# Kernel tuning notes

Measured on AMD Instinct MI355X. Metric: run time of the kernel, lower is better.

Reference implementation:

```python
import jax, jax.numpy as jnp
import numpy as np

N, D = 1024, 256


def setup_inputs() -> dict:
    key = jax.random.key(0)
    k1, k2, k3, k4, k5 = jax.random.split(key, 5)
    s1 = 1.0 / np.sqrt(2 * D)  # fan_in of first linear
    s2 = 1.0 / np.sqrt(D)      # fan_in of second linear
    return {
        "nodes": jax.random.normal(k1, (N, D), dtype=jnp.float32),
        "W1": jax.random.normal(k2, (D, 2 * D), dtype=jnp.float32) * s1,
        "b1": jax.random.normal(k3, (D,), dtype=jnp.float32) * s1,
        "W2": jax.random.normal(k4, (1, D), dtype=jnp.float32) * s2,
        "b2": jax.random.normal(k5, (1,), dtype=jnp.float32) * s2,
    }


def reference(nodes, W1, b1, W2, b2):
    # Original: pair = cat([n_i, n_j], -1); A = sigmoid(Linear2(relu(Linear1(pair))))
    # Algebraically: Linear1(cat(n_i, n_j)) = n_i @ Wa^T + n_j @ Wb^T + b1
    d = nodes.shape[1]
    Wa, Wb = W1[:, :d], W1[:, d:]
    a = nodes @ Wa.T  # (N, D) row-side projection
    b = nodes @ Wb.T  # (N, D) col-side projection
    h = jax.nn.relu(a[:, None, :] + b[None, :, :] + b1)  # (N, N, D)
    logits = jnp.einsum("ijd,d->ij", h, W2[0]) + b2[0]   # (N, N)
    return jax.nn.sigmoid(logits)
```

## Files before the change

### kernel.cpp

```cpp
#include <hip/hip_runtime.h>
#include <math.h>

#define N_NODES 1024
#define DIM     256

__global__ __launch_bounds__(256) void k1_gemm(
    const float* __restrict__ nodes, const float* __restrict__ W1,
    const float* __restrict__ b1, float* __restrict__ At, float* __restrict__ Bt)
{
    __shared__ float nt[64][34];
    __shared__ float wa[64][34];
    __shared__ float wb[64][34];

    const int i0 = (blockIdx.x & 31) * 32;
    const int d0 = (blockIdx.x >> 5) * 32;
    const int t  = threadIdx.x;
    const int tx = t & 15;
    const int ty = t >> 4;

    float aA00=0.f,aA01=0.f,aA10=0.f,aA11=0.f;
    float aB00=0.f,aB01=0.f,aB10=0.f,aB11=0.f;

    const int r = t >> 3;
    const int c = (t & 7) * 8;

    for (int k0 = 0; k0 < DIM; k0 += 64) {
        const float* sn = nodes + (i0 + r) * DIM + k0 + c;
        float4 n0 = *(const float4*)(sn);
        float4 n1 = *(const float4*)(sn + 4);
        const float* sa = W1 + (d0 + r) * (2 * DIM) + k0 + c;
        float4 a0 = *(const float4*)(sa);
        float4 a1 = *(const float4*)(sa + 4);
        const float* sb = sa + DIM;
        float4 q0 = *(const float4*)(sb);
        float4 q1 = *(const float4*)(sb + 4);

        __syncthreads();

        nt[c+0][r]=n0.x; nt[c+1][r]=n0.y; nt[c+2][r]=n0.z; nt[c+3][r]=n0.w;
        nt[c+4][r]=n1.x; nt[c+5][r]=n1.y; nt[c+6][r]=n1.z; nt[c+7][r]=n1.w;
        wa[c+0][r]=a0.x; wa[c+1][r]=a0.y; wa[c+2][r]=a0.z; wa[c+3][r]=a0.w;
        wa[c+4][r]=a1.x; wa[c+5][r]=a1.y; wa[c+6][r]=a1.z; wa[c+7][r]=a1.w;
        wb[c+0][r]=q0.x; wb[c+1][r]=q0.y; wb[c+2][r]=q0.z; wb[c+3][r]=q0.w;
        wb[c+4][r]=q1.x; wb[c+5][r]=q1.y; wb[c+6][r]=q1.z; wb[c+7][r]=q1.w;

        __syncthreads();

        #pragma unroll 16
        for (int k = 0; k < 64; ++k) {
            float2 av = *(const float2*)&nt[k][tx*2];
            float2 pv = *(const float2*)&wa[k][ty*2];
            float2 qv = *(const float2*)&wb[k][ty*2];
            aA00 += av.x*pv.x; aA01 += av.x*pv.y;
            aA10 += av.y*pv.x; aA11 += av.y*pv.y;
            aB00 += av.x*qv.x; aB01 += av.x*qv.y;
            aB10 += av.y*qv.x; aB11 += av.y*qv.y;
        }
    }

    const int i = i0 + tx*2;
    const int d = d0 + ty*2;
    const float bb0 = b1[d], bb1 = b1[d+1];
    At[(d  )*N_NODES + i  ] = aA00 + bb0;
    At[(d+1)*N_NODES + i  ] = aA01 + bb1;
    At[(d  )*N_NODES + i+1] = aA10 + bb0;
    At[(d+1)*N_NODES + i+1] = aA11 + bb1;
    Bt[(d  )*N_NODES + i  ] = aB00;
    Bt[(d+1)*N_NODES + i  ] = aB01;
    Bt[(d  )*N_NODES + i+1] = aB10;
    Bt[(d+1)*N_NODES + i+1] = aB11;
}

__global__ __launch_bounds__(256) void k2_pair(
    const float* __restrict__ At, const float* __restrict__ Bt,
    const float* __restrict__ W2, const float* __restrict__ b2,
    float* __restrict__ out)
{
    __shared__ float As[64][68];
    __shared__ float Bs[64][68];
    __shared__ float w2s[DIM];

    const int i0 = (blockIdx.x & 15) * 64;
    const int j0 = (blockIdx.x >> 4) * 64;
    const int t  = threadIdx.x;
    const int tx = t & 15;
    const int ty = t >> 4;

    w2s[t] = W2[t];

    float acc[4][4] = {{0.f,0.f,0.f,0.f},{0.f,0.f,0.f,0.f},
                       {0.f,0.f,0.f,0.f},{0.f,0.f,0.f,0.f}};

    const int r = t >> 2;
    const int c = (t & 3) * 16;

    for (int dc = 0; dc < DIM; dc += 64) {
        const float* sa = At + (dc + r) * N_NODES + i0 + c;
        const float* sb = Bt + (dc + r) * N_NODES + j0 + c;
        float4 va0 = *(const float4*)(sa);
        float4 va1 = *(const float4*)(sa + 4);
        float4 va2 = *(const float4*)(sa + 8);
        float4 va3 = *(const float4*)(sa + 12);
        float4 vb0 = *(const float4*)(sb);
        float4 vb1 = *(const float4*)(sb + 4);
        float4 vb2 = *(const float4*)(sb + 8);
        float4 vb3 = *(const float4*)(sb + 12);

        __syncthreads();

        *(float4*)&As[r][c   ] = va0;
        *(float4*)&As[r][c+ 4] = va1;
        *(float4*)&As[r][c+ 8] = va2;
        *(float4*)&As[r][c+12] = va3;
        *(float4*)&Bs[r][c   ] = vb0;
        *(float4*)&Bs[r][c+ 4] = vb1;
        *(float4*)&Bs[r][c+ 8] = vb2;
        *(float4*)&Bs[r][c+12] = vb3;

        __syncthreads();

        #pragma unroll 16
        for (int k = 0; k < 64; ++k) {
            float4 a4 = *(const float4*)&As[k][ty*4];
            float4 b4 = *(const float4*)&Bs[k][tx*4];
            float  w  = w2s[dc + k];
            acc[0][0] += fmaxf(a4.x + b4.x, 0.f) * w;
            acc[0][1] += fmaxf(a4.x + b4.y, 0.f) * w;
            acc[0][2] += fmaxf(a4.x + b4.z, 0.f) * w;
            acc[0][3] += fmaxf(a4.x + b4.w, 0.f) * w;
            acc[1][0] += fmaxf(a4.y + b4.x, 0.f) * w;
            acc[1][1] += fmaxf(a4.y + b4.y, 0.f) * w;
            acc[1][2] += fmaxf(a4.y + b4.z, 0.f) * w;
            acc[1][3] += fmaxf(a4.y + b4.w, 0.f) * w;
            acc[2][0] += fmaxf(a4.z + b4.x, 0.f) * w;
            acc[2][1] += fmaxf(a4.z + b4.y, 0.f) * w;
            acc[2][2] += fmaxf(a4.z + b4.z, 0.f) * w;
            acc[2][3] += fmaxf(a4.z + b4.w, 0.f) * w;
            acc[3][0] += fmaxf(a4.w + b4.x, 0.f) * w;
            acc[3][1] += fmaxf(a4.w + b4.y, 0.f) * w;
            acc[3][2] += fmaxf(a4.w + b4.z, 0.f) * w;
            acc[3][3] += fmaxf(a4.w + b4.w, 0.f) * w;
        }
    }

    const float bb = b2[0];
    #pragma unroll
    for (int m = 0; m < 4; ++m) {
        float4 o;
        float x0 = acc[m][0] + bb;
        float x1 = acc[m][1] + bb;
        float x2 = acc[m][2] + bb;
        float x3 = acc[m][3] + bb;
        o.x = 1.0f / (1.0f + __expf(-x0));
        o.y = 1.0f / (1.0f + __expf(-x1));
        o.z = 1.0f / (1.0f + __expf(-x2));
        o.w = 1.0f / (1.0f + __expf(-x3));
        *(float4*)&out[(i0 + ty*4 + m) * N_NODES + j0 + tx*4] = o;
    }
}

extern "C" void kernel_launch(void* const* d_in, const int* in_sizes, int n_in,
                              void* d_out, int out_size, void* d_ws, size_t ws_size,
                              hipStream_t stream) {
    const float* nodes = (const float*)d_in[0];
    const float* W1    = (const float*)d_in[1];
    const float* b1    = (const float*)d_in[2];
    const float* W2    = (const float*)d_in[3];
    const float* b2    = (const float*)d_in[4];
    float* out = (float*)d_out;

    float* At = (float*)d_ws;
    float* Bt = At + DIM * N_NODES;

    k1_gemm<<<256, 256, 0, stream>>>(nodes, W1, b1, At, Bt);
    k2_pair<<<256, 256, 0, stream>>>(At, Bt, W2, b2, out);
}
```

Before: 102.2 us.

## Rewrite pair kernel with packed-FP32 inline asm and direct global loads

The pair kernel drops its shared-memory staging and barriers and reads At/Bt columns straight from global memory (L1/L2), with smaller 2x4 per-thread tiles and 32x64 blocks. The grid doubles to 512 blocks to fill more CUs. Inline asm issues v_pk_add_f32 and v_pk_fma_f32 so two adds and two FMAs go out per instruction, cutting the VALU issue count of the add-relu-FMA inner loop. The cost is lower register-level reuse per thread and more global/cache traffic per FLOP.

Measured after the change: 150.5 us. +47.2%, slower.

```diff
diff --git a/kernel.cpp b/kernel.cpp
--- a/kernel.cpp
+++ b/kernel.cpp
@@ -3,6 +3,33 @@
 
 #define N_NODES 1024
 #define DIM     256
+
+typedef float f32x2 __attribute__((ext_vector_type(2)));
+typedef float f32x4 __attribute__((ext_vector_type(4)));
+
+__device__ __forceinline__ f32x2 pk_add_blo(f32x2 a, f32x2 b) {
+    f32x2 d;
+    asm("v_pk_add_f32 %0, %1, %2 op_sel:[0,0] op_sel_hi:[0,1]"
+        : "=v"(d) : "v"(a), "v"(b));
+    return d;
+}
+__device__ __forceinline__ f32x2 pk_add_bhi(f32x2 a, f32x2 b) {
+    f32x2 d;
+    asm("v_pk_add_f32 %0, %1, %2 op_sel:[1,0] op_sel_hi:[1,1]"
+        : "=v"(d) : "v"(a), "v"(b));
+    return d;
+}
+__device__ __forceinline__ void pk_fma_wlo(f32x2& acc, f32x2 h, f32x2 w) {
+    asm("v_pk_fma_f32 %0, %1, %2, %0 op_sel:[0,0,0] op_sel_hi:[1,0,1]"
+        : "+v"(acc) : "v"(h), "v"(w));
+}
+__device__ __forceinline__ void pk_fma_whi(f32x2& acc, f32x2 h, f32x2 w) {
+    asm("v_pk_fma_f32 %0, %1, %2, %0 op_sel:[0,1,0] op_sel_hi:[1,1,1]"
+        : "+v"(acc) : "v"(h), "v"(w));
+}
+__device__ __forceinline__ f32x2 relu2(f32x2 x) {
+    return __builtin_elementwise_max(x, (f32x2)0.0f);
+}
 
 __global__ __launch_bounds__(256) void k1_gemm(
     const float* __restrict__ nodes, const float* __restrict__ W1,
@@ -71,92 +98,64 @@
     Bt[(d+1)*N_NODES + i+1] = aB11;
 }
 
-__global__ __launch_bounds__(256) void k2_pair(
+__global__ __launch_bounds__(256, 2) void k2_pair(
     const float* __restrict__ At, const float* __restrict__ Bt,
     const float* __restrict__ W2, const float* __restrict__ b2,
     float* __restrict__ out)
 {
-    __shared__ float As[64][68];
-    __shared__ float Bs[64][68];
-    __shared__ float w2s[DIM];
-
-    const int i0 = (blockIdx.x & 15) * 64;
-    const int j0 = (blockIdx.x >> 4) * 64;
+    const int i0 = (blockIdx.x & 31) * 32;
+    const int j0 = (blockIdx.x >> 5) * 64;
     const int t  = threadIdx.x;
     const int tx = t & 15;
     const int ty = t >> 4;
 
-    w2s[t] = W2[t];
+    const float* __restrict__ Ar = At + i0 + ty*2;
+    const float* __restrict__ Br = Bt + j0 + tx*4;
 
-    float acc[4][4] = {{0.f,0.f,0.f,0.f},{0.f,0.f,0.f,0.f},
-                       {0.f,0.f,0.f,0.f},{0.f,0.f,0.f,0.f}};
+    f32x2 acc00 = {0.f,0.f}, acc01 = {0.f,0.f};
+    f32x2 acc10 = {0.f,0.f}, acc11 = {0.f,0.f};
 
-    const int r = t >> 2;
-    const int c = (t & 3) * 16;
+    #pragma unroll 4
+    for (int d = 0; d < DIM; d += 2) {
+        f32x2 wp = *(const f32x2*)(W2 + d);
 
-    for (int dc = 0; dc < DIM; dc += 64) {
-        const float* sa = At + (dc + r) * N_NODES + i0 + c;
-        const float* sb = Bt + (dc + r) * N_NODES + j0 + c;
-        float4 va0 = *(const float4*)(sa);
-        float4 va1 = *(const float4*)(sa + 4);
-        float4 va2 = *(const float4*)(sa + 8);
-        float4 va3 = *(const float4*)(sa + 12);
-        float4 vb0 = *(const float4*)(sb);
-        float4 vb1 = *(const float4*)(sb + 4);
-        float4 vb2 = *(const float4*)(sb + 8);
-        float4 vb3 = *(const float4*)(sb + 12);
-
-        __syncthreads();
-
-        *(float4*)&As[r][c   ] = va0;
-        *(float4*)&As[r][c+ 4] = va1;
-        *(float4*)&As[r][c+ 8] = va2;
-        *(float4*)&As[r][c+12] = va3;
-        *(float4*)&Bs[r][c   ] = vb0;
-        *(float4*)&Bs[r][c+ 4] = vb1;
-        *(float4*)&Bs[r][c+ 8] = vb2;
-        *(float4*)&Bs[r][c+12] = vb3;
-
-        __syncthreads();
-
-        #pragma unroll 16
-        for (int k = 0; k < 64; ++k) {
-            float4 a4 = *(const float4*)&As[k][ty*4];
-            float4 b4 = *(const float4*)&Bs[k][tx*4];
-            float  w  = w2s[dc + k];
-            acc[0][0] += fmaxf(a4.x + b4.x, 0.f) * w;
-            acc[0][1] += fmaxf(a4.x + b4.y, 0.f) * w;
-            acc[0][2] += fmaxf(a4.x + b4.z, 0.f) * w;
-            acc[0][3] += fmaxf(a4.x + b4.w, 0.f) * w;
-            acc[1][0] += fmaxf(a4.y + b4.x, 0.f) * w;
-            acc[1][1] += fmaxf(a4.y + b4.y, 0.f) * w;
-            acc[1][2] += fmaxf(a4.y + b4.z, 0.f) * w;
-            acc[1][3] += fmaxf(a4.y + b4.w, 0.f) * w;
-            acc[2][0] += fmaxf(a4.z + b4.x, 0.f) * w;
-            acc[2][1] += fmaxf(a4.z + b4.y, 0.f) * w;
-            acc[2][2] += fmaxf(a4.z + b4.z, 0.f) * w;
-            acc[2][3] += fmaxf(a4.z + b4.w, 0.f) * w;
-            acc[3][0] += fmaxf(a4.w + b4.x, 0.f) * w;
-            acc[3][1] += fmaxf(a4.w + b4.y, 0.f) * w;
-            acc[3][2] += fmaxf(a4.w + b4.z, 0.f) * w;
-            acc[3][3] += fmaxf(a4.w + b4.w, 0.f) * w;
+        {
+            f32x2 a2 = *(const f32x2*)(Ar + d*N_NODES);
+            f32x4 b4 = *(const f32x4*)(Br + d*N_NODES);
+            f32x2 b01 = __builtin_shufflevector(b4, b4, 0, 1);
+            f32x2 b23 = __builtin_shufflevector(b4, b4, 2, 3);
+            f32x2 h;
+            h = relu2(pk_add_blo(a2, b01)); pk_fma_wlo(acc00, h, wp);
+            h = relu2(pk_add_blo(a2, b23)); pk_fma_wlo(acc01, h, wp);
+            h = relu2(pk_add_bhi(a2, b01)); pk_fma_wlo(acc10, h, wp);
+            h = relu2(pk_add_bhi(a2, b23)); pk_fma_wlo(acc11, h, wp);
+        }
+        {
+            f32x2 a2 = *(const f32x2*)(Ar + (d+1)*N_NODES);
+            f32x4 b4 = *(const f32x4*)(Br + (d+1)*N_NODES);
+            f32x2 b01 = __builtin_shufflevector(b4, b4, 0, 1);
+            f32x2 b23 = __builtin_shufflevector(b4, b4, 2, 3);
+            f32x2 h;
+            h = relu2(pk_add_blo(a2, b01)); pk_fma_whi(acc00, h, wp);
+            h = relu2(pk_add_blo(a2, b23)); pk_fma_whi(acc01, h, wp);
+            h = relu2(pk_add_bhi(a2, b01)); pk_fma_whi(acc10, h, wp);
+            h = relu2(pk_add_bhi(a2, b23)); pk_fma_whi(acc11, h, wp);
         }
     }
 
     const float bb = b2[0];
+    const int r0 = i0 + ty*2;
+    const int c0 = j0 + tx*4;
+
+    f32x4 o0 = { acc00.x + bb, acc00.y + bb, acc01.x + bb, acc01.y + bb };
+    f32x4 o1 = { acc10.x + bb, acc10.y + bb, acc11.x + bb, acc11.y + bb };
     #pragma unroll
-    for (int m = 0; m < 4; ++m) {
-        float4 o;
-        float x0 = acc[m][0] + bb;
-        float x1 = acc[m][1] + bb;
-        float x2 = acc[m][2] + bb;
-        float x3 = acc[m][3] + bb;
-        o.x = 1.0f / (1.0f + __expf(-x0));
-        o.y = 1.0f / (1.0f + __expf(-x1));
-        o.z = 1.0f / (1.0f + __expf(-x2));
-        o.w = 1.0f / (1.0f + __expf(-x3));
-        *(float4*)&out[(i0 + ty*4 + m) * N_NODES + j0 + tx*4] = o;
+    for (int e = 0; e < 4; ++e) {
+        o0[e] = 1.0f / (1.0f + __expf(-o0[e]));
+        o1[e] = 1.0f / (1.0f + __expf(-o1[e]));
     }
+    *(f32x4*)&out[(r0    ) * N_NODES + c0] = o0;
+    *(f32x4*)&out[(r0 + 1) * N_NODES + c0] = o1;
 }
 
 extern "C" void kernel_launch(void* const* d_in, const int* in_sizes, int n_in,
@@ -173,5 +172,5 @@
     float* Bt = At + DIM * N_NODES;
 
     k1_gemm<<<256, 256, 0, stream>>>(nodes, W1, b1, At, Bt);
-    k2_pair<<<256, 256, 0, stream>>>(At, Bt, W2, b2, out);
+    k2_pair<<<512, 256, 0, stream>>>(At, Bt, W2, b2, out);
 }
```
